# Performance work log

Measured on AMD Instinct MI355X. Metric: run time of the kernel, lower is better.

## Reference

```python
import jax, jax.numpy as jnp
import numpy as np
from math import pi

B, L, S, D, H, M, DK, IND, KS = 8, 3072, 3072, 512, 8, 2, 64, 96, 25


def _linear(x, W, b):
    return x @ W + b


def _moving_avg(x, k):
    # Autoformer-style moving average with edge replication, stride 1.  x: [B, T, D]
    pad = (k - 1) // 2
    xp = jnp.concatenate([jnp.repeat(x[:, :1], pad, axis=1), x,
                          jnp.repeat(x[:, -1:], pad, axis=1)], axis=1)
    c = jnp.cumsum(xp, axis=1)
    c = jnp.concatenate([jnp.zeros_like(c[:, :1]), c], axis=1)
    return (c[:, k:] - c[:, :-k]) / k


def _trend_norm(x, g, b):
    # series_decomp(kernel=25): LayerNorm the seasonal part, add back the trend.
    trend = _moving_avg(x, KS)
    seas = x - trend
    mu = jnp.mean(seas, axis=-1, keepdims=True)
    var = jnp.var(seas, axis=-1, keepdims=True)
    return (seas - mu) * jax.lax.rsqrt(var + 1e-5) * g + b + trend


def _quat_attention(q, k, v, q_om, q_th, k_om, k_th):
    # q: [B,Lq,H,E]; k,v: [B,Sk,H,E]; omegas/thetas: [B,*,H,M]
    Bq, Lq, Hh, E = q.shape
    Sk = k.shape[1]
    Mm = q_om.shape[-1]
    qpos = (jnp.arange(Lq, dtype=q.dtype) / Lq)[None, :, None, None]
    kpos = (jnp.arange(Sk, dtype=q.dtype) / Sk)[None, :, None, None]
    Qa = q_om * qpos + q_th
    Ka = k_om * kpos + k_th
    Qc, Qs = jnp.cos(Qa), jnp.sin(Qa)
    Kc, Ks = jnp.cos(Ka), jnp.sin(Ka)
    q0, q1, q2, q3 = jnp.split(q, 4, axis=-1)
    k0, k1, k2, k3 = jnp.split(k, 4, axis=-1)
    op = lambda a, t: jnp.einsum('blhe,blhm->blhme', a, t)
    Qr = jnp.concatenate([op(q0, Qc) - op(q1, Qs), op(q1, Qc) + op(q0, Qs),
                          op(q2, Qc) + op(q3, Qs), op(q3, Qc) - op(q2, Qs)], axis=-1)
    Kr = jnp.concatenate([op(k0, Kc) - op(k2, Ks), op(k1, Kc) - op(k3, Ks),
                          op(k2, Kc) + op(k0, Ks), op(k3, Kc) + op(k1, Ks)], axis=-1)
    scores = jnp.einsum('blhme,bshme->bhls', Qr, Kr) / Mm
    scale = 1.0 / jnp.sqrt(jnp.asarray(E, q.dtype))
    A = jax.nn.softmax(scale * scores, axis=-1)
    return jnp.einsum('bhls,bshd->blhd', A, v)


def _ltr_layer(p, queries, keys, values):
    Bq, Lq, _ = queries.shape
    Sk = keys.shape[1]
    # kernel_size=1 convs == pointwise linears
    q_om = jax.nn.relu(_linear(queries, p['Wqo'], p['bqo'])).reshape(Bq, Lq, H, M)
    k_om = jax.nn.relu(_linear(keys, p['Wko'], p['bko'])).reshape(Bq, Sk, H, M)
    q_th = (jnp.tanh(_linear(queries, p['Wqt'], p['bqt'])) * pi).reshape(Bq, Lq, H, M)
    k_th = (jnp.tanh(_linear(keys, p['Wkt'], p['bkt'])) * pi).reshape(Bq, Sk, H, M)
    q = _linear(queries, p['Wq'], p['bq']).reshape(Bq, Lq, H, DK)
    k = _linear(keys, p['Wk'], p['bk']).reshape(Bq, Sk, H, DK)
    v = _linear(values, p['Wv'], p['bv']).reshape(Bq, Sk, H, DK)
    out = _quat_attention(q, k, v, q_om, q_th, k_om, k_th).reshape(Bq, Lq, H * DK)
    # D-matrix penalty == first-order difference along sequence
    om_pen = jnp.sum(jnp.diff(q_om, axis=1) ** 2) + jnp.sum(jnp.diff(k_om, axis=1) ** 2)
    th_pen = jnp.sum(q_th ** 2) + jnp.sum(k_th ** 2)
    return _linear(out, p['Wo'], p['bo']), om_pen, th_pen


def setup_inputs() -> dict:
    key = jax.random.key(0)
    ks = iter(jax.random.split(key, 32))
    rn = lambda shape, s=1.0: jax.random.normal(next(ks), shape, jnp.float32) * s
    w = 0.03  # ~1/sqrt(d_model)
    return dict(
        queries=rn((B, L, D)), keys=rn((B, S, D)), values=rn((B, S, D)),
        Wq=rn((2, D, D), w), bq=jnp.zeros((2, D), jnp.float32),
        Wk=rn((2, D, D), w), bk=jnp.zeros((2, D), jnp.float32),
        Wv=rn((2, D, D), w), bv=jnp.zeros((2, D), jnp.float32),
        Wqo=rn((2, D, M * H), w), bqo=jnp.zeros((2, M * H), jnp.float32),
        Wko=rn((2, D, M * H), w), bko=jnp.zeros((2, M * H), jnp.float32),
        Wqt=rn((2, D, M * H), w), bqt=jnp.zeros((2, M * H), jnp.float32),
        Wkt=rn((2, D, M * H), w), bkt=jnp.zeros((2, M * H), jnp.float32),
        Wo=rn((2, D, D), w), bo=jnp.zeros((2, D), jnp.float32),
        I=rn((1, IND, D), w),
        ln_g=jnp.ones((D,), jnp.float32), ln_b=jnp.zeros((D,), jnp.float32),
    )


def reference(queries, keys, values, Wq, bq, Wk, bk, Wv, bv, Wqo, bqo, Wko, bko,
              Wqt, bqt, Wkt, bkt, Wo, bo, I, ln_g, ln_b):
    def lp(i):
        return dict(Wq=Wq[i], bq=bq[i], Wk=Wk[i], bk=bk[i], Wv=Wv[i], bv=bv[i],
                    Wqo=Wqo[i], bqo=bqo[i], Wko=Wko[i], bko=bko[i],
                    Wqt=Wqt[i], bqt=bqt[i], Wkt=Wkt[i], bkt=bkt[i],
                    Wo=Wo[i], bo=bo[i])
    Bq = queries.shape[0]
    inducings = jnp.broadcast_to(I, (Bq, IND, D))
    inducings, om1, th1 = _ltr_layer(lp(0), inducings, keys, values)
    inducings = _trend_norm(inducings, ln_g, ln_b)
    out, om2, th2 = _ltr_layer(lp(1), queries, inducings, inducings)
    return out, om1 + om2, th1 + th2
```

## Files before the change

kernel.cpp:

```cpp
#include <hip/hip_runtime.h>
#include <math.h>

#define PI_F 3.14159265358979323846f

namespace {
constexpr int B_ = 8;
constexpr int L_ = 3072;
constexpr int S_ = 3072;
constexpr int H_ = 8;
constexpr int NF = 544;
constexpr int NSC = 8;
constexpr int SCHUNK = S_ / NSC;
}

typedef __attribute__((ext_vector_type(8))) short bf16x8;
typedef __attribute__((ext_vector_type(4))) float f32x4;

__device__ inline f32x4 mfma16(bf16x8 a, bf16x8 b, f32x4 c) {
  return __builtin_amdgcn_mfma_f32_16x16x32_bf16(a, b, c, 0, 0, 0);
}

__device__ inline ushort f2bf(float f) {
  union { float f; unsigned u; } v;
  v.f = f;
  unsigned r = v.u + 0x7FFFu + ((v.u >> 16) & 1u);
  return (ushort)(r >> 16);
}

__device__ inline void gl_lds16(const void* g, void* l) {
  __builtin_amdgcn_global_load_lds(
      (const __attribute__((address_space(1))) unsigned int*)g,
      (__attribute__((address_space(3))) unsigned int*)l, 16, 0, 0);
}

__device__ inline int xcd_swizzle(int flat, int nwg) {
  int q = nwg >> 3, r = nwg & 7;
  int xcd = flat & 7, ix = flat >> 3;
  return (xcd < r ? xcd * (q + 1) : r * (q + 1) + (xcd - r) * q) + ix;
}

__global__ void init_pen(float* pen) {
  if (threadIdx.x < 16) pen[threadIdx.x] = 0.f;
}

__global__ void write_pen(const float* __restrict__ pen, float* __restrict__ out) {
  if (threadIdx.x == 0) out[12582912] = pen[0];
  if (threadIdx.x == 1) out[12582913] = pen[1];
}

__global__ void pack_w(const float* __restrict__ Wm, const float* __restrict__ Wo_,
                       const float* __restrict__ Wt, const float* __restrict__ bm,
                       const float* __restrict__ bo_, const float* __restrict__ bt,
                       float* __restrict__ Wcat, float* __restrict__ bcat) {
  int gid = blockIdx.x * 256 + threadIdx.x;
  if (gid < 512 * 544) {
    int k = gid / 544, n = gid % 544;
    float v;
    if (n < 512) v = Wm[(size_t)k * 512 + n];
    else if (n < 528) v = Wo_[k * 16 + (n - 512)];
    else v = Wt[k * 16 + (n - 528)];
    Wcat[gid] = v;
  }
  if (gid < 544) {
    float v;
    if (gid < 512) v = bm[gid];
    else if (gid < 528) v = bo_[gid - 512];
    else v = bt[gid - 528];
    bcat[gid] = v;
  }
}

__global__ void pack_wt_fused(const float* __restrict__ Wm, const float* __restrict__ Wo_,
                              const float* __restrict__ Wt, const float* __restrict__ bm,
                              const float* __restrict__ bo_, const float* __restrict__ bt,
                              ushort* __restrict__ BT, float* __restrict__ bias) {
  int gid = blockIdx.x * 256 + threadIdx.x;
  if (gid < 640 * 512) {
    int n = gid >> 9, k = gid & 511;
    float v = 0.f;
    if (n < 512) v = Wm[(size_t)k * 512 + n];
    else if (n < 528) v = Wo_[k * 16 + (n - 512)];
    else if (n < 544) v = Wt[k * 16 + (n - 528)];
    BT[gid] = f2bf(v);
  }
  if (gid < 544)
    bias[gid] = (gid < 512) ? bm[gid] : (gid < 528 ? bo_[gid - 512] : bt[gid - 528]);
}

__global__ void pack_wt_plain(const float* __restrict__ W, const float* __restrict__ b,
                              ushort* __restrict__ BT, float* __restrict__ bias) {
  int gid = blockIdx.x * 256 + threadIdx.x;
  if (gid < 512 * 512) {
    int n = gid >> 9, k = gid & 511;
    BT[gid] = f2bf(W[(size_t)k * 512 + n]);
  }
  if (gid < 512) bias[gid] = b[gid];
}

__global__ __launch_bounds__(256)
void cast_bf16(const float* __restrict__ src, ushort* __restrict__ dst, int n8) {
  int gid = blockIdx.x * 256 + threadIdx.x;
  if (gid < n8) {
    float4 a = ((const float4*)src)[(size_t)gid * 2];
    float4 b = ((const float4*)src)[(size_t)gid * 2 + 1];
    ushort u[8] = {f2bf(a.x), f2bf(a.y), f2bf(a.z), f2bf(a.w),
                   f2bf(b.x), f2bf(b.y), f2bf(b.z), f2bf(b.w)};
    ((uint4*)dst)[gid] = *(uint4*)u;
  }
}

__global__ __launch_bounds__(256)
void gemm_bf16_mfma(const ushort* __restrict__ A, const ushort* __restrict__ BT,
                    const float* __restrict__ bias, void* __restrict__ Cv,
                    int ldc, int Nout, int act, int obf) {
  __shared__ ushort As[128][32];
  __shared__ ushort Bs[128][32];
  const int tid = threadIdx.x;
  const int wv = tid >> 6, lane = tid & 63, quad = lane >> 4, col = lane & 15;
  const int wm = wv & 1, wn = wv >> 1;

  const int nwg = gridDim.x * gridDim.y;
  const int flat = blockIdx.y * gridDim.x + blockIdx.x;
  const int nf = xcd_swizzle(flat, nwg);
  const int bx = nf % gridDim.x, by = nf / gridDim.x;
  const int m0 = by * 128, n0 = bx * 128;

  const int srow = lane >> 2;
  const int scol = (lane & 3) * 8;

  f32x4 acc[4][4];
#pragma unroll
  for (int i = 0; i < 4; ++i)
#pragma unroll
    for (int j = 0; j < 4; ++j) {
      f32x4 z = {0.f, 0.f, 0.f, 0.f};
      acc[i][j] = z;
    }

  const ushort* Ag = A + (size_t)(m0 + wv * 32) * 512;
  const ushort* Bg = BT + (size_t)(n0 + wv * 32) * 512;

  for (int k0 = 0; k0 < 512; k0 += 32) {
    __syncthreads();
    gl_lds16(Ag + (size_t)srow * 512 + k0 + scol, &As[wv * 32][0]);
    gl_lds16(Ag + (size_t)(srow + 16) * 512 + k0 + scol, &As[wv * 32 + 16][0]);
    gl_lds16(Bg + (size_t)srow * 512 + k0 + scol, &Bs[wv * 32][0]);
    gl_lds16(Bg + (size_t)(srow + 16) * 512 + k0 + scol, &Bs[wv * 32 + 16][0]);
    __syncthreads();
    bf16x8 av[4], bv[4];
#pragma unroll
    for (int mi = 0; mi < 4; ++mi)
      av[mi] = *(const bf16x8*)&As[wm * 64 + mi * 16 + col][quad * 8];
#pragma unroll
    for (int ni = 0; ni < 4; ++ni)
      bv[ni] = *(const bf16x8*)&Bs[wn * 64 + ni * 16 + col][quad * 8];
#pragma unroll
    for (int mi = 0; mi < 4; ++mi)
#pragma unroll
      for (int ni = 0; ni < 4; ++ni)
        acc[mi][ni] = mfma16(av[mi], bv[ni], acc[mi][ni]);
  }

  float* Cf = (float*)Cv;
  ushort* Cu = (ushort*)Cv;
#pragma unroll
  for (int mi = 0; mi < 4; ++mi) {
#pragma unroll
    for (int ni = 0; ni < 4; ++ni) {
      int n = n0 + wn * 64 + ni * 16 + col;
      if (n >= Nout) continue;
      float bs = bias[n];
#pragma unroll
      for (int r = 0; r < 4; ++r) {
        int m = m0 + wm * 64 + mi * 16 + quad * 4 + r;
        float v = acc[mi][ni][r] + bs;
        if (act && n >= 512) v = (n < 528) ? fmaxf(v, 0.f) : tanhf(v) * PI_F;
        if (obf) Cu[(size_t)m * ldc + n] = f2bf(v);
        else Cf[(size_t)m * ldc + n] = v;
      }
    }
  }
}

__global__ __launch_bounds__(256)
void gemm_k512(const float* __restrict__ A, const float* __restrict__ W,
               const float* __restrict__ bias, float* __restrict__ C,
               int M, int N, int act) {
  __shared__ float As[16][68];
  __shared__ float Ws_[16][68];
  const int tid = threadIdx.x;
  const int tx = tid & 15, ty = tid >> 4;
  const int m0 = blockIdx.y * 64, n0 = blockIdx.x * 64;

  float acc[4][4];
#pragma unroll
  for (int i = 0; i < 4; ++i)
#pragma unroll
    for (int j = 0; j < 4; ++j) acc[i][j] = 0.f;

  const int arow = tid >> 2;
  const int acol4 = (tid & 3) * 4;
  const int wrow = tid >> 4;
  const int wcol4 = (tid & 15) * 4;

  for (int k0 = 0; k0 < 512; k0 += 16) {
    float4 av = make_float4(0.f, 0.f, 0.f, 0.f);
    int gm = m0 + arow;
    if (gm < M) av = *(const float4*)(A + (size_t)gm * 512 + k0 + acol4);
    As[acol4 + 0][arow] = av.x;
    As[acol4 + 1][arow] = av.y;
    As[acol4 + 2][arow] = av.z;
    As[acol4 + 3][arow] = av.w;
    float4 wv;
    int gn = n0 + wcol4;
    if (gn + 3 < N) {
      wv = *(const float4*)(W + (size_t)(k0 + wrow) * N + gn);
    } else {
      float tmp[4] = {0.f, 0.f, 0.f, 0.f};
      for (int u = 0; u < 4; ++u)
        if (gn + u < N) tmp[u] = W[(size_t)(k0 + wrow) * N + gn + u];
      wv = make_float4(tmp[0], tmp[1], tmp[2], tmp[3]);
    }
    *(float4*)&Ws_[wrow][wcol4] = wv;
    __syncthreads();
#pragma unroll
    for (int k = 0; k < 16; ++k) {
      float4 a4 = *(const float4*)&As[k][ty * 4];
      float4 b4 = *(const float4*)&Ws_[k][tx * 4];
      float a[4] = {a4.x, a4.y, a4.z, a4.w};
      float b[4] = {b4.x, b4.y, b4.z, b4.w};
#pragma unroll
      for (int i = 0; i < 4; ++i)
#pragma unroll
        for (int j = 0; j < 4; ++j) acc[i][j] = fmaf(a[i], b[j], acc[i][j]);
    }
    __syncthreads();
  }

#pragma unroll
  for (int i = 0; i < 4; ++i) {
    int gm = m0 + ty * 4 + i;
    if (gm >= M) continue;
#pragma unroll
    for (int j = 0; j < 4; ++j) {
      int gn = n0 + tx * 4 + j;
      if (gn >= N) continue;
      float v = acc[i][j] + bias[gn];
      if (act && gn >= 512) v = (gn < 528) ? fmaxf(v, 0.f) : tanhf(v) * PI_F;
      C[(size_t)gm * N + gn] = v;
    }
  }
}

__global__ __launch_bounds__(256)
void build_qr0(const float* __restrict__ QF0, ushort* __restrict__ Qr0bf) {
  const int l = blockIdx.x;
  const float* row = QF0 + (size_t)l * NF;
  __shared__ float2 trig[8][2];
  const int tid = threadIdx.x;
  if (tid < 16) {
    int h = tid >> 1, m = tid & 1;
    float om = row[512 + h * 2 + m], th = row[528 + h * 2 + m];
    float qa = fmaf(om, (float)l / 96.f, th);
    trig[h][m] = make_float2(cosf(qa), sinf(qa));
  }
  __syncthreads();
  for (int idx = tid; idx < 1024; idx += 256) {
    int h = idx >> 7, d = idx & 127;
    int m = d >> 6, r = d & 63, c = r >> 4, e = r & 15;
    float qc = row[h * 64 + c * 16 + e];
    float qp = row[h * 64 + (c ^ 1) * 16 + e];
    float2 tg = trig[h][m];
    float sgn = (c == 0 || c == 3) ? -1.f : 1.f;
    Qr0bf[((size_t)h * 96 + l) * 128 + d] = f2bf(fmaf(qc, tg.x, sgn * qp * tg.y));
  }
}

__global__ __launch_bounds__(256)
void build_kr0(const float* __restrict__ KF0, ushort* __restrict__ Kr0) {
  const int rs = blockIdx.x;
  const int b = rs / S_, s = rs - b * S_;
  const float* row = KF0 + (size_t)rs * NF;
  __shared__ float2 trig[8][2];
  const int tid = threadIdx.x;
  if (tid < 16) {
    int h = tid >> 1, m = tid & 1;
    float om = row[512 + h * 2 + m], th = row[528 + h * 2 + m];
    float ka = fmaf(om, (float)s * (1.f / (float)S_), th);
    trig[h][m] = make_float2(cosf(ka), sinf(ka));
  }
  __syncthreads();
  for (int idx = tid; idx < 512; idx += 256) {
    int h = idx >> 6, d = (idx & 63) * 2;
    int m = d >> 6, r = d & 63, c = r >> 4, e = r & 15;
    const float* rh = row + h * 64;
    float2 kc = *(const float2*)(rh + c * 16 + e);
    float2 kp = *(const float2*)(rh + (c ^ 2) * 16 + e);
    float2 tg = trig[h][m];
    float sgn = (c < 2) ? -1.f : 1.f;
    ushort2 u;
    u.x = f2bf(fmaf(kc.x, tg.x, sgn * kp.x * tg.y));
    u.y = f2bf(fmaf(kc.y, tg.x, sgn * kp.y * tg.y));
    *(ushort2*)&Kr0[(((size_t)(b * 8 + h)) * S_ + s) * 128 + d] = u;
  }
}

__global__ __launch_bounds__(256)
void build_vt0(const ushort* __restrict__ V0b, ushort* __restrict__ Vt0) {
  const int st = blockIdx.x, h = blockIdx.y, b = blockIdx.z;
  const int s0 = st * 64;
  const int tid = threadIdx.x;
  __shared__ ushort T[64][68];
  for (int idx = tid; idx < 4096; idx += 256) {
    int s = idx >> 6, d = idx & 63;
    T[d][s] = V0b[((size_t)(b * S_ + s0 + s)) * 512 + h * 64 + d];
  }
  __syncthreads();
  for (int idx = tid; idx < 2048; idx += 256) {
    int d = idx >> 5, s2 = (idx & 31) * 2;
    ushort2 u = *(const ushort2*)&T[d][s2];
    *(ushort2*)&Vt0[(((size_t)(b * 8 + h)) * 64 + d) * S_ + s0 + s2] = u;
  }
}

__global__ __launch_bounds__(256)
void build_kr1(const float* __restrict__ KF1, ushort* __restrict__ Kr1b) {
  const int rs = blockIdx.x;
  const int b = rs / 96, s = rs % 96;
  const float* row = KF1 + (size_t)rs * NF;
  __shared__ float2 trig[8][2];
  const int tid = threadIdx.x;
  if (tid < 16) {
    int h = tid >> 1, m = tid & 1;
    float om = row[512 + h * 2 + m], th = row[528 + h * 2 + m];
    float ka = fmaf(om, (float)s / 96.f, th);
    trig[h][m] = make_float2(cosf(ka), sinf(ka));
  }
  __syncthreads();
  for (int idx = tid; idx < 512; idx += 256) {
    int h = idx >> 6, d = (idx & 63) * 2;
    int m = d >> 6, r = d & 63, c = r >> 4, e = r & 15;
    const float* rh = row + h * 64;
    float2 kc = *(const float2*)(rh + c * 16 + e);
    float2 kp = *(const float2*)(rh + (c ^ 2) * 16 + e);
    float2 tg = trig[h][m];
    float sgn = (c < 2) ? -1.f : 1.f;
    ushort2 u;
    u.x = f2bf(fmaf(kc.x, tg.x, sgn * kp.x * tg.y));
    u.y = f2bf(fmaf(kc.y, tg.x, sgn * kp.y * tg.y));
    *(ushort2*)&Kr1b[(((size_t)(b * 8 + h)) * 96 + s) * 128 + d] = u;
  }
}

__global__ __launch_bounds__(256)
void build_qr1(const float* __restrict__ QF1, ushort* __restrict__ Qr1) {
  const int rl = blockIdx.x;
  const int b = rl / L_, l = rl - b * L_;
  const float* row = QF1 + (size_t)rl * NF;
  __shared__ float2 trig[8][2];
  const int tid = threadIdx.x;
  if (tid < 16) {
    int h = tid >> 1, m = tid & 1;
    float om = row[512 + h * 2 + m], th = row[528 + h * 2 + m];
    float qa = fmaf(om, (float)l * (1.f / (float)L_), th);
    trig[h][m] = make_float2(cosf(qa), sinf(qa));
  }
  __syncthreads();
  for (int idx = tid; idx < 512; idx += 256) {
    int h = idx >> 6, d = (idx & 63) * 2;
    int m = d >> 6, r = d & 63, c = r >> 4, e = r & 15;
    const float* rh = row + h * 64;
    float2 qc = *(const float2*)(rh + c * 16 + e);
    float2 qp = *(const float2*)(rh + (c ^ 1) * 16 + e);
    float2 tg = trig[h][m];
    float sgn = (c == 0 || c == 3) ? -1.f : 1.f;
    ushort2 u;
    u.x = f2bf(fmaf(qc.x, tg.x, sgn * qp.x * tg.y));
    u.y = f2bf(fmaf(qc.y, tg.x, sgn * qp.y * tg.y));
    *(ushort2*)&Qr1[(((size_t)(b * 8 + h)) * L_ + l) * 128 + d] = u;
  }
}

__global__ __launch_bounds__(256)
void build_vt1(const float* __restrict__ V1, ushort* __restrict__ Vt1) {
  const int h = blockIdx.x, b = blockIdx.y;
  const int tid = threadIdx.x;
  __shared__ ushort T[64][104];
  for (int idx = tid; idx < 96 * 64; idx += 256) {
    int s = idx >> 6, d = idx & 63;
    T[d][s] = f2bf(V1[(size_t)(b * 96 + s) * 512 + h * 64 + d]);
  }
  __syncthreads();
  for (int idx = tid; idx < 64 * 12; idx += 256) {
    int d = idx / 12, c8 = (idx % 12) * 8;
    *(uint4*)&Vt1[(((size_t)(b * 8 + h)) * 64 + d) * 96 + c8] = *(const uint4*)&T[d][c8];
  }
}

__global__ __launch_bounds__(256)
void attn0_mfma(const ushort* __restrict__ Kr0, const ushort* __restrict__ Vt0,
                const ushort* __restrict__ Qr0bf, float* __restrict__ accP,
                float* __restrict__ sumP) {
  const int sc = blockIdx.x, h = blockIdx.y, b = blockIdx.z;
  const int tid = threadIdx.x;
  const int wv = tid >> 6, lane = tid & 63, quad = lane >> 4, col = lane & 15;

  __shared__ __align__(16) ushort Qs[96][136];
  __shared__ __align__(16) ushort Ps[96][72];
  __shared__ float rowsum[96];

  const int s0g = sc * SCHUNK;
  const ushort* Kb = Kr0 + ((size_t)(b * 8 + h) * S_ + s0g) * 128;
  const ushort* Vb = Vt0 + ((size_t)(b * 8 + h)) * 64 * S_ + s0g;

  bf16x8 bk[6][4];
#pragma unroll
  for (int t = 0; t < 6; ++t) {
    const ushort* Kt = Kb + ((size_t)(t * 64 + wv * 16 + col)) * 128;
#pragma unroll
    for (int k = 0; k < 4; ++k) bk[t][k] = *(const bf16x8*)(Kt + k * 32 + quad * 8);
  }
  bf16x8 bv[6][2];
  {
    const ushort* Vt = Vb + ((size_t)(wv * 16 + col)) * S_;
#pragma unroll
    for (int t = 0; t < 6; ++t) {
      bv[t][0] = *(const bf16x8*)(Vt + t * 64 + quad * 8);
      bv[t][1] = *(const bf16x8*)(Vt + t * 64 + 32 + quad * 8);
    }
  }
  __builtin_amdgcn_sched_barrier(0);

  const ushort* Qg = Qr0bf + (size_t)h * 96 * 128;
  for (int idx = tid; idx < 96 * 16; idx += 256) {
    int l = idx >> 4, c8 = (idx & 15) * 8;
    *(uint4*)&Qs[l][c8] = *(const uint4*)(Qg + (size_t)l * 128 + c8);
  }
  if (tid < 96) rowsum[tid] = 0.f;

  f32x4 oacc[6];
#pragma unroll
  for (int i = 0; i < 6; ++i) {
    f32x4 z = {0.f, 0.f, 0.f, 0.f};
    oacc[i] = z;
  }

  __syncthreads();

#pragma unroll
  for (int t = 0; t < 6; ++t) {
    f32x4 sacc[6];
#pragma unroll
    for (int mt = 0; mt < 6; ++mt) {
      f32x4 z = {0.f, 0.f, 0.f, 0.f};
      sacc[mt] = z;
#pragma unroll
      for (int k = 0; k < 4; ++k) {
        bf16x8 a = *(const bf16x8*)&Qs[mt * 16 + col][k * 32 + quad * 8];
        sacc[mt] = mfma16(a, bk[t][k], sacc[mt]);
      }
    }
#pragma unroll
    for (int mt = 0; mt < 6; ++mt) {
      float pr[4];
#pragma unroll
      for (int r = 0; r < 4; ++r) {
        float p = __expf(sacc[mt][r] * 0.0625f);
        pr[r] = p;
        Ps[mt * 16 + quad * 4 + r][wv * 16 + col] = f2bf(p);
      }
#pragma unroll
      for (int r = 0; r < 4; ++r) {
#pragma unroll
        for (int off = 1; off < 16; off <<= 1) pr[r] += __shfl_xor(pr[r], off);
      }
      if (col == 0) {
#pragma unroll
        for (int r = 0; r < 4; ++r)
          atomicAdd(&rowsum[mt * 16 + quad * 4 + r], pr[r]);
      }
    }
    __syncthreads();
#pragma unroll
    for (int mt = 0; mt < 6; ++mt) {
      bf16x8 a0 = *(const bf16x8*)&Ps[mt * 16 + col][quad * 8];
      oacc[mt] = mfma16(a0, bv[t][0], oacc[mt]);
      bf16x8 a1 = *(const bf16x8*)&Ps[mt * 16 + col][32 + quad * 8];
      oacc[mt] = mfma16(a1, bv[t][1], oacc[mt]);
    }
    __syncthreads();
  }
  const size_t pbase = (((size_t)(b * 8 + h)) * NSC + sc) * 96;
#pragma unroll
  for (int mt = 0; mt < 6; ++mt) {
#pragma unroll
    for (int r = 0; r < 4; ++r) {
      int l = mt * 16 + quad * 4 + r;
      accP[(pbase + l) * 64 + wv * 16 + col] = oacc[mt][r];
    }
  }
  if (tid < 96) sumP[pbase + tid] = rowsum[tid];
}

__global__ __launch_bounds__(256)
void attn0_stage2(const float* __restrict__ accP, const float* __restrict__ sumP,
                  float* __restrict__ attn0) {
  const int l = blockIdx.x, b = blockIdx.y;
  const int tid = threadIdx.x;
  for (int e = tid; e < 512; e += 256) {
    int h = e >> 6, d = e & 63;
    size_t base = ((size_t)(b * 8 + h)) * NSC * 96;
    float num = 0.f, den = 0.f;
    for (int scv = 0; scv < NSC; ++scv) {
      size_t pb = base + (size_t)scv * 96 + l;
      num += accP[pb * 64 + d];
      den += sumP[pb];
    }
    attn0[((size_t)(b * 96 + l)) * 512 + e] = num / den;
  }
}

__global__ __launch_bounds__(256)
void trend_norm(const float* __restrict__ y, const float* __restrict__ g,
                const float* __restrict__ be, float* __restrict__ outp) {
  const int t = blockIdx.x, b = blockIdx.y;
  const int tid = threadIdx.x;
  __shared__ float red[256];
  __shared__ float red2[256];
  float seas[2], trend[2];
  float lsum = 0.f, lsum2 = 0.f;
#pragma unroll
  for (int u = 0; u < 2; ++u) {
    int d = tid + u * 256;
    float tr = 0.f;
    for (int j = -12; j <= 12; ++j) {
      int tt = t + j;
      tt = tt < 0 ? 0 : (tt > 95 ? 95 : tt);
      tr += y[((size_t)(b * 96 + tt)) * 512 + d];
    }
    tr *= (1.f / 25.f);
    float x = y[((size_t)(b * 96 + t)) * 512 + d];
    float se = x - tr;
    seas[u] = se;
    trend[u] = tr;
    lsum += se;
    lsum2 += se * se;
  }
  red[tid] = lsum;
  red2[tid] = lsum2;
  __syncthreads();
  for (int off = 128; off > 0; off >>= 1) {
    if (tid < off) {
      red[tid] += red[tid + off];
      red2[tid] += red2[tid + off];
    }
    __syncthreads();
  }
  float mu = red[0] / 512.f;
  float var = red2[0] / 512.f - mu * mu;
  float rs = rsqrtf(var + 1e-5f);
#pragma unroll
  for (int u = 0; u < 2; ++u) {
    int d = tid + u * 256;
    outp[((size_t)(b * 96 + t)) * 512 + d] = (seas[u] - mu) * rs * g[d] + be[d] + trend[u];
  }
}

__global__ __launch_bounds__(256)
void penalty(const float* __restrict__ base, int R, int nb, float mult,
             float* __restrict__ pen) {
  const int tid = threadIdx.x;
  size_t gid = (size_t)blockIdx.x * 256 + tid;
  size_t total = (size_t)nb * R * 16;
  float omv = 0.f, thv = 0.f;
  if (gid < total) {
    int j = (int)(gid & 15);
    size_t row = gid >> 4;
    int s = (int)(row % R);
    const float* r0 = base + row * NF;
    float th = r0[528 + j];
    thv = th * th;
    if (s < R - 1) {
      float d = r0[NF + 512 + j] - r0[512 + j];
      omv = d * d;
    }
  }
  __shared__ float ro[256], rt[256];
  ro[tid] = omv;
  rt[tid] = thv;
  __syncthreads();
  for (int off = 128; off > 0; off >>= 1) {
    if (tid < off) {
      ro[tid] += ro[tid + off];
      rt[tid] += rt[tid + off];
    }
    __syncthreads();
  }
  if (tid == 0) {
    atomicAdd(pen + 0, mult * ro[0]);
    atomicAdd(pen + 1, mult * rt[0]);
  }
}

__global__ __launch_bounds__(256)
void attn1_mfma(const ushort* __restrict__ Qr1, const ushort* __restrict__ Kr1b,
                const ushort* __restrict__ Vt1, ushort* __restrict__ attn1) {
  const int nwg = gridDim.x * gridDim.y * gridDim.z;
  const int flat = (blockIdx.z * gridDim.y + blockIdx.y) * gridDim.x + blockIdx.x;
  const int nf = xcd_swizzle(flat, nwg);
  const int lt = nf % gridDim.x;
  const int rest = nf / gridDim.x;
  const int h = rest % gridDim.y, b = rest / gridDim.y;
  const int l0 = lt * 64;
  const int tid = threadIdx.x;
  const int wv = tid >> 6, lane = tid & 63, quad = lane >> 4, col = lane & 15;

  __shared__ __align__(16) ushort Ps[64][104];

  const ushort* Qg = Qr1 + ((size_t)(b * 8 + h) * L_ + l0) * 128;
  const ushort* Kg = Kr1b + (size_t)(b * 8 + h) * 96 * 128;
  const ushort* Vg = Vt1 + (size_t)(b * 8 + h) * 64 * 96;

  bf16x8 aq[4];
#pragma unroll
  for (int k = 0; k < 4; ++k)
    aq[k] = *(const bf16x8*)(Qg + ((size_t)(wv * 16 + col)) * 128 + k * 32 + quad * 8);
  bf16x8 bk[6][4];
#pragma unroll
  for (int nt = 0; nt < 6; ++nt)
#pragma unroll
    for (int k = 0; k < 4; ++k)
      bk[nt][k] =
          *(const bf16x8*)(Kg + ((size_t)(nt * 16 + col)) * 128 + k * 32 + quad * 8);
  bf16x8 bv[4][3];
#pragma unroll
  for (int nt = 0; nt < 4; ++nt)
#pragma unroll
    for (int kt = 0; kt < 3; ++kt)
      bv[nt][kt] =
          *(const bf16x8*)(Vg + ((size_t)(nt * 16 + col)) * 96 + kt * 32 + quad * 8);
  __builtin_amdgcn_sched_barrier(0);

  f32x4 sacc[6];
#pragma unroll
  for (int nt = 0; nt < 6; ++nt) {
    f32x4 z = {0.f, 0.f, 0.f, 0.f};
    sacc[nt] = z;
#pragma unroll
    for (int k = 0; k < 4; ++k) sacc[nt] = mfma16(aq[k], bk[nt][k], sacc[nt]);
  }
  float rsum[4] = {0.f, 0.f, 0.f, 0.f};
#pragma unroll
  for (int nt = 0; nt < 6; ++nt) {
#pragma unroll
    for (int r = 0; r < 4; ++r) {
      float p = __expf(sacc[nt][r] * 0.0625f);
      Ps[wv * 16 + quad * 4 + r][nt * 16 + col] = f2bf(p);
      rsum[r] += p;
    }
  }
#pragma unroll
  for (int r = 0; r < 4; ++r) {
#pragma unroll
    for (int off = 1; off < 16; off <<= 1) rsum[r] += __shfl_xor(rsum[r], off);
  }
  __syncthreads();
  bf16x8 ap[3];
#pragma unroll
  for (int kt = 0; kt < 3; ++kt)
    ap[kt] = *(const bf16x8*)&Ps[wv * 16 + col][kt * 32 + quad * 8];
  f32x4 oacc[4];
#pragma unroll
  for (int nt = 0; nt < 4; ++nt) {
    f32x4 z = {0.f, 0.f, 0.f, 0.f};
    oacc[nt] = z;
#pragma unroll
    for (int kt = 0; kt < 3; ++kt) oacc[nt] = mfma16(ap[kt], bv[nt][kt], oacc[nt]);
  }
  float inv[4];
#pragma unroll
  for (int r = 0; r < 4; ++r) inv[r] = 1.f / rsum[r];
#pragma unroll
  for (int nt = 0; nt < 4; ++nt) {
#pragma unroll
    for (int r = 0; r < 4; ++r) {
      int l = wv * 16 + quad * 4 + r;
      attn1[(size_t)(b * L_ + l0 + l) * 512 + h * 64 + nt * 16 + col] =
          f2bf(oacc[nt][r] * inv[r]);
    }
  }
}

extern "C" void kernel_launch(void* const* d_in, const int* in_sizes, int n_in,
                              void* d_out, int out_size, void* d_ws, size_t ws_size,
                              hipStream_t stream) {
  (void)in_sizes; (void)n_in; (void)out_size; (void)ws_size;
  const float* queries = (const float*)d_in[0];
  const float* keys = (const float*)d_in[1];
  const float* values = (const float*)d_in[2];
  const float* Wq = (const float*)d_in[3];
  const float* bq = (const float*)d_in[4];
  const float* Wk = (const float*)d_in[5];
  const float* bk = (const float*)d_in[6];
  const float* Wv = (const float*)d_in[7];
  const float* bv = (const float*)d_in[8];
  const float* Wqo = (const float*)d_in[9];
  const float* bqo = (const float*)d_in[10];
  const float* Wko = (const float*)d_in[11];
  const float* bko = (const float*)d_in[12];
  const float* Wqt = (const float*)d_in[13];
  const float* bqt = (const float*)d_in[14];
  const float* Wkt = (const float*)d_in[15];
  const float* bkt = (const float*)d_in[16];
  const float* Wo = (const float*)d_in[17];
  const float* bo = (const float*)d_in[18];
  const float* I = (const float*)d_in[19];
  const float* ln_g = (const float*)d_in[20];
  const float* ln_b = (const float*)d_in[21];
  float* out = (float*)d_out;

  float* ws = (float*)d_ws;
  size_t off = 0;
  auto alloc = [&](size_t n) {
    float* p = ws + off;
    off += (n + 3) & ~(size_t)3;
    return p;
  };
  auto allocU = [&](size_t n) { return (ushort*)alloc((n + 1) / 2); };

  float* WCAT0Q = alloc(512 * 544);
  float* WCAT1K = alloc(512 * 544);
  float* BCAT0Q = alloc(544);
  float* BCAT1K = alloc(544);
  ushort* BT0K = allocU(640 * 512);
  ushort* BT1Q = allocU(640 * 512);
  ushort* BTV0 = allocU(512 * 512);
  ushort* BTO1 = allocU(512 * 512);
  float* B0K = alloc(544);
  float* B1Q = alloc(544);
  float* BV0 = alloc(512);
  float* BO1 = alloc(512);
  float* pen = alloc(16);
  float* QF0 = alloc(96 * 544);
  ushort* Qr0bf = allocU(8 * 96 * 128);
  float* KF0 = alloc((size_t)24576 * 544);
  float* V0 = alloc((size_t)24576 * 512);
  float* attn0 = alloc(768 * 512);
  float* y0 = alloc(768 * 512);
  float* xind = alloc(768 * 512);
  float* KF1 = alloc(768 * 544);
  float* V1 = alloc(768 * 512);
  ushort* Kr1b = allocU((size_t)64 * 96 * 128);
  ushort* Vt1 = allocU((size_t)64 * 64 * 96);
  float* accP = alloc((size_t)64 * NSC * 96 * 64);
  float* sumP = alloc((size_t)64 * NSC * 96);
  ushort* XB1 = allocU((size_t)24576 * 512);
  ushort* XB2 = allocU((size_t)24576 * 512);
  ushort* Kr0U = XB1;
  ushort* Vt0U = allocU((size_t)64 * 64 * S_);
  float* QF1 = KF0;
  ushort* V0b = (ushort*)V0;
  ushort* Qr1U = (ushort*)V0;

  init_pen<<<1, 64, 0, stream>>>(pen);
  const int packBlocks = (512 * 544 + 255) / 256;
  pack_w<<<packBlocks, 256, 0, stream>>>(Wq, Wqo, Wqt, bq, bqo, bqt, WCAT0Q, BCAT0Q);
  pack_w<<<packBlocks, 256, 0, stream>>>(Wk + 262144, Wko + 8192, Wkt + 8192,
                                         bk + 512, bko + 16, bkt + 16, WCAT1K, BCAT1K);
  pack_wt_fused<<<(640 * 512 + 255) / 256, 256, 0, stream>>>(
      Wk, Wko, Wkt, bk, bko, bkt, BT0K, B0K);
  pack_wt_fused<<<(640 * 512 + 255) / 256, 256, 0, stream>>>(
      Wq + 262144, Wqo + 8192, Wqt + 8192, bq + 512, bqo + 16, bqt + 16, BT1Q, B1Q);
  pack_wt_plain<<<(512 * 512 + 255) / 256, 256, 0, stream>>>(Wv, bv, BTV0, BV0);
  pack_wt_plain<<<(512 * 512 + 255) / 256, 256, 0, stream>>>(Wo + 262144, bo + 512,
                                                             BTO1, BO1);
  const int castBlocks = (24576 * 512 / 8 + 255) / 256;
  cast_bf16<<<castBlocks, 256, 0, stream>>>(keys, XB1, 24576 * 512 / 8);
  cast_bf16<<<castBlocks, 256, 0, stream>>>(values, XB2, 24576 * 512 / 8);

  gemm_bf16_mfma<<<dim3(5, 192), 256, 0, stream>>>(XB1, BT0K, B0K, KF0, 544, 544, 1, 0);
  gemm_bf16_mfma<<<dim3(4, 192), 256, 0, stream>>>(XB2, BTV0, BV0, V0b, 512, 512, 0, 1);
  gemm_k512<<<dim3(9, 2), 256, 0, stream>>>(I, WCAT0Q, BCAT0Q, QF0, 96, 544, 1);
  build_qr0<<<96, 256, 0, stream>>>(QF0, Qr0bf);
  penalty<<<(96 * 16 + 255) / 256, 256, 0, stream>>>(QF0, 96, 1, 8.f, pen);
  penalty<<<(24576 * 16 + 255) / 256, 256, 0, stream>>>(KF0, 3072, 8, 1.f, pen);
  build_kr0<<<24576, 256, 0, stream>>>(KF0, Kr0U);
  build_vt0<<<dim3(48, 8, 8), 256, 0, stream>>>(V0b, Vt0U);
  attn0_mfma<<<dim3(8, 8, 8), 256, 0, stream>>>(Kr0U, Vt0U, Qr0bf, accP, sumP);
  attn0_stage2<<<dim3(96, 8), 256, 0, stream>>>(accP, sumP, attn0);
  gemm_k512<<<dim3(8, 12), 256, 0, stream>>>(attn0, Wo, bo, y0, 768, 512, 0);
  trend_norm<<<dim3(96, 8), 256, 0, stream>>>(y0, ln_g, ln_b, xind);

  gemm_k512<<<dim3(9, 12), 256, 0, stream>>>(xind, WCAT1K, BCAT1K, KF1, 768, 544, 1);
  gemm_k512<<<dim3(8, 12), 256, 0, stream>>>(xind, Wv + 262144, bv + 512, V1, 768, 512, 0);
  build_kr1<<<768, 256, 0, stream>>>(KF1, Kr1b);
  build_vt1<<<dim3(8, 8), 256, 0, stream>>>(V1, Vt1);
  penalty<<<(768 * 16 + 255) / 256, 256, 0, stream>>>(KF1, 96, 8, 1.f, pen);
  cast_bf16<<<castBlocks, 256, 0, stream>>>(queries, XB1, 24576 * 512 / 8);
  gemm_bf16_mfma<<<dim3(5, 192), 256, 0, stream>>>(XB1, BT1Q, B1Q, QF1, 544, 544, 1, 0);
  penalty<<<(24576 * 16 + 255) / 256, 256, 0, stream>>>(QF1, 3072, 8, 1.f, pen);
  build_qr1<<<24576, 256, 0, stream>>>(QF1, Qr1U);
  attn1_mfma<<<dim3(48, 8, 8), 256, 0, stream>>>(Qr1U, Kr1b, Vt1, XB2);
  gemm_bf16_mfma<<<dim3(4, 192), 256, 0, stream>>>(XB2, BTO1, BO1, out, 512, 512, 0, 0);
  write_pen<<<1, 64, 0, stream>>>(pen, out);
}
```

Baseline: 797.2 us.

## Double-buffer GEMM LDS tiles and stage attention K/V and output through LDS

The bf16 GEMM now keeps two LDS buffers and loads the next K-slice while MFMAs run on the current one, leaving one barrier per iteration instead of two. The attn1 kernel loads K and V cooperatively into LDS with 16-byte loads instead of each wave pulling all fragments into registers, which lowers register pressure. Its output is written to LDS and then stored as coalesced 16-byte rows instead of scattered 2-byte stores. These changes add LDS use and extra barriers, which could reduce occupancy.

```diff
diff --git a/kernel.cpp b/kernel.cpp
--- a/kernel.cpp
+++ b/kernel.cpp
@@ -113,8 +113,8 @@
 void gemm_bf16_mfma(const ushort* __restrict__ A, const ushort* __restrict__ BT,
                     const float* __restrict__ bias, void* __restrict__ Cv,
                     int ldc, int Nout, int act, int obf) {
-  __shared__ ushort As[128][32];
-  __shared__ ushort Bs[128][32];
+  __shared__ ushort As[2][128][32];
+  __shared__ ushort Bs[2][128][32];
   const int tid = threadIdx.x;
   const int wv = tid >> 6, lane = tid & 63, quad = lane >> 4, col = lane & 15;
   const int wm = wv & 1, wn = wv >> 1;
@@ -140,25 +140,37 @@
   const ushort* Ag = A + (size_t)(m0 + wv * 32) * 512;
   const ushort* Bg = BT + (size_t)(n0 + wv * 32) * 512;
 
-  for (int k0 = 0; k0 < 512; k0 += 32) {
-    __syncthreads();
-    gl_lds16(Ag + (size_t)srow * 512 + k0 + scol, &As[wv * 32][0]);
-    gl_lds16(Ag + (size_t)(srow + 16) * 512 + k0 + scol, &As[wv * 32 + 16][0]);
-    gl_lds16(Bg + (size_t)srow * 512 + k0 + scol, &Bs[wv * 32][0]);
-    gl_lds16(Bg + (size_t)(srow + 16) * 512 + k0 + scol, &Bs[wv * 32 + 16][0]);
-    __syncthreads();
+  auto stage = [&](int bb, int k0) {
+    gl_lds16(Ag + (size_t)srow * 512 + k0 + scol, &As[bb][wv * 32][0]);
+    gl_lds16(Ag + (size_t)(srow + 16) * 512 + k0 + scol, &As[bb][wv * 32 + 16][0]);
+    gl_lds16(Bg + (size_t)srow * 512 + k0 + scol, &Bs[bb][wv * 32][0]);
+    gl_lds16(Bg + (size_t)(srow + 16) * 512 + k0 + scol, &Bs[bb][wv * 32 + 16][0]);
+  };
+
+  stage(0, 0);
+  asm volatile("s_waitcnt vmcnt(0)" ::: "memory");
+  __builtin_amdgcn_s_barrier();
+  __builtin_amdgcn_sched_barrier(0);
+
+  for (int i = 0; i < 16; ++i) {
+    const int cur = i & 1;
+    if (i < 15) stage(cur ^ 1, (i + 1) * 32);
     bf16x8 av[4], bv[4];
 #pragma unroll
     for (int mi = 0; mi < 4; ++mi)
-      av[mi] = *(const bf16x8*)&As[wm * 64 + mi * 16 + col][quad * 8];
+      av[mi] = *(const bf16x8*)&As[cur][wm * 64 + mi * 16 + col][quad * 8];
 #pragma unroll
     for (int ni = 0; ni < 4; ++ni)
-      bv[ni] = *(const bf16x8*)&Bs[wn * 64 + ni * 16 + col][quad * 8];
+      bv[ni] = *(const bf16x8*)&Bs[cur][wn * 64 + ni * 16 + col][quad * 8];
 #pragma unroll
     for (int mi = 0; mi < 4; ++mi)
 #pragma unroll
       for (int ni = 0; ni < 4; ++ni)
         acc[mi][ni] = mfma16(av[mi], bv[ni], acc[mi][ni]);
+    __builtin_amdgcn_sched_barrier(0);
+    asm volatile("s_waitcnt vmcnt(0)" ::: "memory");
+    __builtin_amdgcn_s_barrier();
+    __builtin_amdgcn_sched_barrier(0);
   }
 
   float* Cf = (float*)Cv;
@@ -615,31 +627,28 @@
   const int tid = threadIdx.x;
   const int wv = tid >> 6, lane = tid & 63, quad = lane >> 4, col = lane & 15;
 
+  __shared__ __align__(16) ushort Ks[96][136];
+  __shared__ __align__(16) ushort Vs[64][104];
   __shared__ __align__(16) ushort Ps[64][104];
+  ushort(*Os)[72] = reinterpret_cast<ushort(*)[72]>(&Ks[0][0]);
 
   const ushort* Qg = Qr1 + ((size_t)(b * 8 + h) * L_ + l0) * 128;
   const ushort* Kg = Kr1b + (size_t)(b * 8 + h) * 96 * 128;
   const ushort* Vg = Vt1 + (size_t)(b * 8 + h) * 64 * 96;
 
+  for (int idx = tid; idx < 96 * 16; idx += 256) {
+    int r = idx >> 4, c8 = (idx & 15) * 8;
+    *(uint4*)&Ks[r][c8] = *(const uint4*)(Kg + (size_t)r * 128 + c8);
+  }
+  for (int idx = tid; idx < 64 * 12; idx += 256) {
+    int r = idx / 12, c8 = (idx % 12) * 8;
+    *(uint4*)&Vs[r][c8] = *(const uint4*)(Vg + (size_t)r * 96 + c8);
+  }
   bf16x8 aq[4];
 #pragma unroll
   for (int k = 0; k < 4; ++k)
     aq[k] = *(const bf16x8*)(Qg + ((size_t)(wv * 16 + col)) * 128 + k * 32 + quad * 8);
-  bf16x8 bk[6][4];
-#pragma unroll
-  for (int nt = 0; nt < 6; ++nt)
-#pragma unroll
-    for (int k = 0; k < 4; ++k)
-      bk[nt][k] =
-          *(const bf16x8*)(Kg + ((size_t)(nt * 16 + col)) * 128 + k * 32 + quad * 8);
-  bf16x8 bv[4][3];
-#pragma unroll
-  for (int nt = 0; nt < 4; ++nt)
-#pragma unroll
-    for (int kt = 0; kt < 3; ++kt)
-      bv[nt][kt] =
-          *(const bf16x8*)(Vg + ((size_t)(nt * 16 + col)) * 96 + kt * 32 + quad * 8);
-  __builtin_amdgcn_sched_barrier(0);
+  __syncthreads();
 
   f32x4 sacc[6];
 #pragma unroll
@@ -647,7 +656,10 @@
     f32x4 z = {0.f, 0.f, 0.f, 0.f};
     sacc[nt] = z;
 #pragma unroll
-    for (int k = 0; k < 4; ++k) sacc[nt] = mfma16(aq[k], bk[nt][k], sacc[nt]);
+    for (int k = 0; k < 4; ++k) {
+      bf16x8 bkf = *(const bf16x8*)&Ks[nt * 16 + col][k * 32 + quad * 8];
+      sacc[nt] = mfma16(aq[k], bkf, sacc[nt]);
+    }
   }
   float rsum[4] = {0.f, 0.f, 0.f, 0.f};
 #pragma unroll
@@ -675,7 +687,10 @@
     f32x4 z = {0.f, 0.f, 0.f, 0.f};
     oacc[nt] = z;
 #pragma unroll
-    for (int kt = 0; kt < 3; ++kt) oacc[nt] = mfma16(ap[kt], bv[nt][kt], oacc[nt]);
+    for (int kt = 0; kt < 3; ++kt) {
+      bf16x8 bvf = *(const bf16x8*)&Vs[nt * 16 + col][kt * 32 + quad * 8];
+      oacc[nt] = mfma16(ap[kt], bvf, oacc[nt]);
+    }
   }
   float inv[4];
 #pragma unroll
@@ -684,10 +699,14 @@
   for (int nt = 0; nt < 4; ++nt) {
 #pragma unroll
     for (int r = 0; r < 4; ++r) {
-      int l = wv * 16 + quad * 4 + r;
-      attn1[(size_t)(b * L_ + l0 + l) * 512 + h * 64 + nt * 16 + col] =
-          f2bf(oacc[nt][r] * inv[r]);
-    }
+      Os[wv * 16 + quad * 4 + r][nt * 16 + col] = f2bf(oacc[nt][r] * inv[r]);
+    }
+  }
+  __syncthreads();
+  for (int idx = tid; idx < 64 * 8; idx += 256) {
+    int l = idx >> 3, c8 = (idx & 7) * 8;
+    *(uint4*)(attn1 + (size_t)(b * L_ + l0 + l) * 512 + h * 64 + c8) =
+        *(const uint4*)&Os[l][c8];
   }
 }
 
```

After: 794.7 us. No clear change (-0.3%).
